# Kernel optimization log

Measured on AMD Instinct MI355X. Metric: run time of the kernel, lower is better.

The kernel has to match this reference:

```python
import jax, jax.numpy as jnp
import numpy as np

B, S, D = 4, 2048, 1024
N_NEURONS, K = 512, 8
N_BASIS, R = 32, 512
N_HEADS = 8
D_HEAD = R // N_HEADS


def setup_inputs() -> dict:
    key = jax.random.key(0)
    ks = jax.random.split(key, 8)
    x = jax.random.normal(ks[0], (B, S, D), dtype=jnp.float32)
    W_router = jax.random.normal(ks[1], (N_NEURONS, D), dtype=jnp.float32) / np.sqrt(D)
    recipe_Q = jax.random.normal(ks[2], (N_NEURONS, N_BASIS), dtype=jnp.float32)
    recipe_K = jax.random.normal(ks[3], (N_NEURONS, N_BASIS), dtype=jnp.float32)
    recipe_V = jax.random.normal(ks[4], (N_NEURONS, N_BASIS), dtype=jnp.float32)
    # orthonormal basis: QR of random [D, R] per basis slot (buffer, not trained)
    raw = jax.random.normal(ks[5], (N_BASIS, D, R), dtype=jnp.float32)
    basis = jax.vmap(lambda m: jnp.linalg.qr(m)[0])(raw)  # [N_BASIS, D, R]
    W_o = jax.random.normal(ks[6], (D, R), dtype=jnp.float32) / np.sqrt(R)
    mask = jnp.tril(jnp.ones((S, S), dtype=jnp.int32))[None, None]  # [1,1,S,S] causal
    mask = jnp.broadcast_to(mask, (B, 1, S, S))
    return {"x": x, "W_router": W_router, "recipe_Q": recipe_Q, "recipe_K": recipe_K,
            "recipe_V": recipe_V, "basis": basis, "W_o": W_o, "mask": mask}


def reference(x, W_router, recipe_Q, recipe_K, recipe_V, basis, W_o, mask):
    # routing: pick top-k neurons per token
    scores = jnp.einsum('bsd,nd->bsn', x, W_router)            # [B,S,N_NEURONS]
    topk_scores, topk_idx = jax.lax.top_k(scores, K)            # [B,S,K]
    weights = jax.nn.softmax(topk_scores, axis=-1)              # [B,S,K]

    def token_recipe(recipe):
        g = recipe[topk_idx]                                    # [B,S,K,N_BASIS]
        r = jnp.einsum('bskn,bsk->bsn', g, weights)             # [B,S,N_BASIS]
        return jax.nn.softmax(r, axis=-1)

    tQ = token_recipe(recipe_Q)
    tK = token_recipe(recipe_K)
    tV = token_recipe(recipe_V)

    # shared basis projection of x, reused for Q/K/V (same math as
    # W = einsum('bsn,ndr->bsdr'); Q = einsum('bsd,bsdr->bsr'))
    P = jnp.einsum('bsd,ndr->bsnr', x, basis)                   # [B,S,N_BASIS,R]
    Q = jnp.einsum('bsnr,bsn->bsr', P, tQ)
    Kt = jnp.einsum('bsnr,bsn->bsr', P, tK)
    V = jnp.einsum('bsnr,bsn->bsr', P, tV)

    def heads(t):
        return t.reshape(B, S, N_HEADS, D_HEAD).transpose(0, 2, 1, 3)  # [B,H,S,dh]

    Qh, Kh, Vh = heads(Q), heads(Kt), heads(V)
    attn = jnp.einsum('bhqd,bhkd->bhqk', Qh, Kh) / np.sqrt(D_HEAD)
    attn = jnp.where(mask == 0, jnp.float32(-1e30), attn)
    attn = jax.nn.softmax(attn, axis=-1)                        # dropout p: eval/no-op
    out = jnp.einsum('bhqk,bhkd->bhqd', attn, Vh)
    out = out.transpose(0, 2, 1, 3).reshape(B, S, R)
    attn_out = jnp.einsum('bsr,dr->bsd', out, W_o)
    return attn_out, topk_idx, weights
```

## Files before the change

### kernel.cpp

```cpp
#include <hip/hip_runtime.h>
#include <math.h>
#include <stdint.h>


typedef __attribute__((ext_vector_type(4))) float f32x4;
typedef __attribute__((ext_vector_type(8))) short s16x8;
typedef __attribute__((ext_vector_type(4))) short s16x4;
typedef __attribute__((ext_vector_type(4))) int i32x4;
typedef __attribute__((ext_vector_type(8))) int i32x8;

#define DEV __device__ __forceinline__

DEV short f2bf(float f){
  union { float f; unsigned u; } c; c.f = f;
  unsigned u = c.u;
  unsigned r = (u + 0x7fffu + ((u >> 16) & 1u)) >> 16;
  return (short)r;
}
DEV float bf2f(short s){
  union { unsigned u; float f; } c; c.u = ((unsigned)(unsigned short)s) << 16;
  return c.f;
}
DEV unsigned char f2e4m3(float f){
  union { float f; unsigned u; } c; c.f = f;
  unsigned u = c.u;
  unsigned sign = (u >> 24) & 0x80u;
  unsigned a = u & 0x7fffffffu;
  if (a >= 0x43e00000u) return (unsigned char)(sign | 0x7Eu);
  if (a < 0x3c800000u){
    union { unsigned u; float f; } d; d.u = a;
    int q = (int)(d.f * 512.0f + 0.5f);
    return (unsigned char)(sign | (unsigned)q);
  }
  unsigned m = a & 0x7fffffu;
  unsigned e = (a >> 23) - 120u;
  unsigned keep = m >> 20;
  unsigned rest = m & 0xFFFFFu;
  if (rest > 0x80000u || (rest == 0x80000u && (keep & 1u))){
    keep++;
    if (keep == 8u){ keep = 0; e++; }
  }
  if (e >= 16u || (e == 15u && keep == 7u)) return (unsigned char)(sign | 0x7Eu);
  return (unsigned char)(sign | (e << 3) | keep);
}

typedef __attribute__((address_space(3))) void lds_vt;
typedef const __attribute__((address_space(1))) void g_vt;
DEV void gload16(const void* g, void* lds){
  __builtin_amdgcn_global_load_lds((g_vt*)g, (lds_vt*)lds, 16, 0, 0);
}

DEV int gslot(int c){ return (c < 4) ? (c << 1) : (((c - 4) << 1) + 1); }

__global__ void k_conv_w(const float* __restrict__ Wo, const float* __restrict__ Wrt,
                         short* __restrict__ Wob, short* __restrict__ Wrtb){
  int i = blockIdx.x*256 + threadIdx.x;
  const float* src = (i < 131072) ? Wo : Wrt;
  short* dst = (i < 131072) ? Wob : Wrtb;
  int j = (i < 131072) ? i : (i - 131072);
  float4 v = ((const float4*)src)[j];
  s16x4 o; o[0]=f2bf(v.x); o[1]=f2bf(v.y); o[2]=f2bf(v.z); o[3]=f2bf(v.w);
  ((s16x4*)dst)[j] = o;
}

__global__ void k_conv_x(const float* __restrict__ in, short* __restrict__ Xb, char* __restrict__ Xf8){
  int t = blockIdx.x*256 + threadIdx.x;
  size_t d = (size_t)t * 16;
  const float4* s = (const float4*)(in + d);
  float vals[16];
  #pragma unroll
  for (int q=0;q<4;q++){ float4 v = s[q]; vals[q*4]=v.x; vals[q*4+1]=v.y; vals[q*4+2]=v.z; vals[q*4+3]=v.w; }
  s16x8 ob0, ob1;
  unsigned long long v0 = 0, v1 = 0;
  #pragma unroll
  for (int e=0;e<8;e++){
    ob0[e] = f2bf(vals[e]);
    ob1[e] = f2bf(vals[8+e]);
    v0 |= ((unsigned long long)f2e4m3(vals[e]))   << (8*e);
    v1 |= ((unsigned long long)f2e4m3(vals[8+e])) << (8*e);
  }
  *(s16x8*)(Xb + d) = ob0;
  *(s16x8*)(Xb + d + 8) = ob1;
  int c = t & 7;
  char* dst = Xf8 + (d & ~(size_t)127) + (gslot(c) << 4);
  *(unsigned long long*)dst = v0;
  *(unsigned long long*)(dst + 8) = v1;
}

__global__ __launch_bounds__(256) void k_conv_basis8(const float* __restrict__ basis, char* __restrict__ B2f){
  __shared__ float tile[64][65];
  int tid = threadIdx.x;
  int r0 = blockIdx.x<<6, d0 = blockIdx.y<<6, n = blockIdx.z;
  const float* src = basis + ((size_t)n*1024 + d0)*512 + r0;
  for (int i = tid; i < 4096; i += 256){ int dd = i>>6, rr = i&63; tile[dd][rr] = src[(size_t)dd*512 + rr]; }
  __syncthreads();
  int rr = tid >> 2, j = tid & 3;
  unsigned long long v0 = 0, v1 = 0;
  #pragma unroll
  for (int e=0;e<8;e++){
    v0 |= ((unsigned long long)f2e4m3(tile[j*16+e][rr]))   << (8*e);
    v1 |= ((unsigned long long)f2e4m3(tile[j*16+8+e][rr])) << (8*e);
  }
  int c = j + ((d0 >> 4) & 4);
  char* dst = B2f + ((size_t)(r0+rr)*32 + n)*1024 + (size_t)(d0 & ~127) + (gslot(c) << 4);
  *(unsigned long long*)dst = v0;
  *(unsigned long long*)(dst + 8) = v1;
}

__global__ __launch_bounds__(256) void k_gemm_c32(
    const short* __restrict__ A, const short* __restrict__ Bt, int Kd, int Mblk,
    float* __restrict__ C, int ldc)
{
  __shared__ char smem[32768];
  short* Asm = (short*)smem;
  short* Bsm = (short*)(smem + 16384);
  int tid = threadIdx.x, lane = tid & 63, w = tid >> 6;
  int wr = w >> 1, wc = w & 1;
  int nwg = gridDim.x, bid = blockIdx.x;
  int sid = (bid & 7) * (nwg >> 3) + (bid >> 3);
  int row0 = (sid % Mblk) << 7;
  int col0 = (sid / Mblk) << 7;
  f32x4 acc[4][4];
  #pragma unroll
  for (int m=0;m<4;m++)
    #pragma unroll
    for (int nf=0;nf<4;nf++)
      #pragma unroll
      for (int e=0;e<4;e++) acc[m][nf][e] = 0.f;
  int lr8 = lane >> 3;
  int lk_sw = (((lane & 7) ^ (lane >> 3)) << 3);
  for (int k0 = 0; k0 < Kd; k0 += 64){
    #pragma unroll
    for (int i=0;i<4;i++){
      int chunk = (w<<2) + i;
      int r = (chunk<<3) + lr8;
      gload16(A  + (size_t)(row0 + r)*Kd + k0 + lk_sw, smem + chunk*1024);
      gload16(Bt + (size_t)(col0 + r)*Kd + k0 + lk_sw, smem + 16384 + chunk*1024);
    }
    __syncthreads();
    #pragma unroll
    for (int kk=0; kk<2; kk++){
      int csw = (kk*32 + ((lane>>4)<<3)) ^ ((lane & 7) << 3);
      s16x8 af[4], bfr[4];
      #pragma unroll
      for (int m=0;m<4;m++)
        af[m] = *(const s16x8*)(Asm + ((wr*64 + m*16 + (lane&15))*64 + csw));
      #pragma unroll
      for (int nf=0;nf<4;nf++)
        bfr[nf] = *(const s16x8*)(Bsm + ((wc*64 + nf*16 + (lane&15))*64 + csw));
      #pragma unroll
      for (int m=0;m<4;m++)
        #pragma unroll
        for (int nf=0;nf<4;nf++)
          acc[m][nf] = __builtin_amdgcn_mfma_f32_16x16x32_bf16(af[m], bfr[nf], acc[m][nf], 0, 0, 0);
    }
    __syncthreads();
  }
  #pragma unroll
  for (int m=0;m<4;m++)
    #pragma unroll
    for (int nf=0;nf<4;nf++)
      #pragma unroll
      for (int e=0;e<4;e++){
        int tok = wr*64 + m*16 + ((lane>>4)<<2) + e;
        int col = wc*64 + nf*16 + (lane&15);
        C[(size_t)(row0+tok)*ldc + col0 + col] = acc[m][nf][e];
      }
}

#define STAGE_A(slotOff, arow0, tkt) do{ \
  int _t = (tkt) < 7 ? (tkt) : 7; \
  int _r = tid>>3, _g = tid&7; \
  gload16(B2f + (size_t)(row0 + (arow0) + _r)*1024 + (_t<<7) + ((_g ^ (_r&7))<<4), \
          smem + (slotOff) + (_r<<7) + (_g<<4)); \
}while(0)

#define STAGE_B(slotOff, trow0, tkt) do{ \
  int _t = (tkt) < 7 ? (tkt) : 7; \
  int _r = tid>>3, _g = tid&7; \
  gload16(Xf8 + (size_t)(col0 + (trow0) + _r)*1024 + (_t<<7) + ((_g ^ (_r&7))<<4), \
          smem + (slotOff) + (_r<<7) + (_g<<4)); \
  gload16(Xf8 + (size_t)(col0 + (trow0) + 64 + _r)*1024 + (_t<<7) + ((_g ^ (_r&7))<<4), \
          smem + (slotOff) + ((64+_r)<<7) + (_g<<4)); \
}while(0)

#define LD_AF(dst, base) \
  _Pragma("unroll") \
  for (int mi=0;mi<2;mi++){ \
    const char* _p = (base) + (wm*32 + mi*16 + l15)*128; \
    i32x4* _h = (i32x4*)&dst[mi]; \
    _h[0] = *(const i32x4*)(_p + ((ga0 ^ l7)<<4)); \
    _h[1] = *(const i32x4*)(_p + ((ga1 ^ l7)<<4)); \
  }

#define LD_BF(dst, base) \
  _Pragma("unroll") \
  for (int ni=0;ni<2;ni++){ \
    const char* _p = (base) + (wn*32 + ni*16 + l15)*128; \
    i32x4* _h = (i32x4*)&dst[ni]; \
    _h[0] = *(const i32x4*)(_p + ((ga0 ^ l7)<<4)); \
    _h[1] = *(const i32x4*)(_p + ((ga1 ^ l7)<<4)); \
  }

#define VMC(N) asm volatile("s_waitcnt vmcnt(" #N ")" ::: "memory")
#define PBAR() do{ __builtin_amdgcn_sched_barrier(0); __builtin_amdgcn_s_barrier(); }while(0)

#define MFMAP(Q, AF, BF) do{ \
  __builtin_amdgcn_s_setprio(1); \
  _Pragma("unroll") \
  for (int mi=0;mi<2;mi++) \
    _Pragma("unroll") \
    for (int ni=0;ni<2;ni++) \
      acc[Q][mi][ni] = __builtin_amdgcn_mfma_scale_f32_16x16x128_f8f6f4( \
          AF[mi], BF[ni], acc[Q][mi][ni], 0, 0, 0, 0x7f7f7f7f, 0, 0x7f7f7f7f); \
  __builtin_amdgcn_s_setprio(0); \
}while(0)

__global__ __launch_bounds__(512, 4) void k_pgemm8(
    const char* __restrict__ B2f, const char* __restrict__ Xf8,
    const float* __restrict__ tQp, const float* __restrict__ tKp, const float* __restrict__ tVp,
    short* __restrict__ Qb, short* __restrict__ Kb, short* __restrict__ Vt)
{
  extern __shared__ char smem[];
  int tid = threadIdx.x, lane = tid & 63, wid = tid >> 6;
  int wm = wid >> 2, wn = wid & 3;
  int l15 = lane & 15, l7 = lane & 7, g16 = lane >> 4;
  int ga0 = (g16 < 2) ? (g16 << 2) : (((g16 - 2) << 2) + 1);
  int ga1 = ga0 + 2;
  int bid = blockIdx.x;
  int xcd = bid & 7, lid = bid >> 3;
  int t_tile = (xcd << 2) + (lid & 3);
  int c_tile = lid >> 2;
  int row0 = c_tile << 7;
  int col0 = t_tile << 8;

  f32x4 acc[4][2][2];
  #pragma unroll
  for (int q=0;q<4;q++)
    #pragma unroll
    for (int mi=0;mi<2;mi++)
      #pragma unroll
      for (int ni=0;ni<2;ni++)
        #pragma unroll
        for (int e=0;e<4;e++) acc[q][mi][ni][e] = 0.f;
  i32x8 af[2], bf[2];

  STAGE_A(0, 0, 0);
  STAGE_B(24576, 0, 0);
  STAGE_A(16384, 64, 0);
  VMC(1);
  PBAR();

  for (int kt = 0; kt < 8; ++kt){
    const char* A0c = smem + ((kt&1)<<13);
    LD_AF(af, A0c);
    LD_BF(bf, smem + 24576);
    STAGE_B(40960, 128, kt);
    VMC(2);
    PBAR();
    MFMAP(0, af, bf);
    LD_AF(af, smem + 16384);
    STAGE_A(((kt+1)&1)<<13, 0, kt+1);
    VMC(1);
    PBAR();
    MFMAP(1, af, bf);
    LD_BF(bf, smem + 40960);
    STAGE_B(24576, 0, kt+1);
    PBAR();
    MFMAP(2, af, bf);
    LD_AF(af, A0c);
    STAGE_A(16384, 64, kt+1);
    VMC(1);
    PBAR();
    MFMAP(3, af, bf);
  }

  VMC(0);
  __syncthreads();
  short* t16 = (short*)smem;
  for (int i = tid; i < 8192; i += 512){
    int tk = i >> 5, n = i & 31;
    t16[tk*36 + n]            = f2bf(tQp[(size_t)col0*32 + i]);
    t16[9216 + tk*36 + n]     = f2bf(tKp[(size_t)col0*32 + i]);
    t16[18432 + tk*36 + n]    = f2bf(tVp[(size_t)col0*32 + i]);
  }
  __syncthreads();
  int g4 = g16 << 2;
  #pragma unroll
  for (int rec=0; rec<3; rec++){
    const short* tb = t16 + rec*9216;
    #pragma unroll
    for (int q=0;q<4;q++){
      int rh = (q==1)||(q==2);
      int ch = q >> 1;
      int r = (c_tile << 2) + rh*2 + wm;
      #pragma unroll
      for (int ni=0;ni<2;ni++){
        int tok = ch*128 + wn*32 + ni*16 + l15;
        s16x4 tlo = *(const s16x4*)(tb + tok*36 + g4);
        s16x4 thi = *(const s16x4*)(tb + tok*36 + 16 + g4);
        float p = 0.f;
        #pragma unroll
        for (int e=0;e<4;e++) p += acc[q][0][ni][e] * bf2f(tlo[e]);
        #pragma unroll
        for (int e=0;e<4;e++) p += acc[q][1][ni][e] * bf2f(thi[e]);
        p += __shfl_xor(p, 16);
        p += __shfl_xor(p, 32);
        if (g16 == rec){
          int gtok = col0 + tok;
          if (rec == 0)      Qb[(size_t)gtok*512 + r] = f2bf(p);
          else if (rec == 1) Kb[(size_t)gtok*512 + r] = f2bf(p);
          else Vt[(((size_t)(gtok>>11)*8 + (r>>6))*64 + (r&63))*2048 + (gtok&2047)] = f2bf(p);
        }
      }
    }
  }
}

__global__ __launch_bounds__(64) void k_router(const float* __restrict__ scores,
    const float* __restrict__ X, const float* __restrict__ W,
    const float* __restrict__ rQ, const float* __restrict__ rK, const float* __restrict__ rV,
    float* __restrict__ tQ, float* __restrict__ tK, float* __restrict__ tV,
    float* __restrict__ oidx, float* __restrict__ ow){
  int token = blockIdx.x; int lane = threadIdx.x;
  const float* srow = scores + (size_t)token*512;
  float v[8];
  #pragma unroll
  for (int j=0;j<8;j++) v[j] = srow[lane + 64*j];
  int myidx = 0x7fffffff;
  #pragma unroll
  for (int k=0;k<16;k++){
    float bm = -INFINITY; int bi = 0x7fffffff;
    #pragma unroll
    for (int j=0;j<8;j++){ if (v[j] > bm) { bm = v[j]; bi = lane + 64*j; } }
    #pragma unroll
    for (int off=32; off>=1; off>>=1){
      float om = __shfl_xor(bm, off); int oi = __shfl_xor(bi, off);
      if (om > bm || (om == bm && oi < bi)) { bm = om; bi = oi; }
    }
    if (lane == k) myidx = bi;
    #pragma unroll
    for (int j=0;j<8;j++) if (lane + 64*j == bi) v[j] = -INFINITY;
  }
  float xr[16];
  {
    const float4* x4 = (const float4*)(X + (size_t)token*1024 + lane*16);
    #pragma unroll
    for (int q=0;q<4;q++){ float4 t = x4[q]; xr[q*4]=t.x; xr[q*4+1]=t.y; xr[q*4+2]=t.z; xr[q*4+3]=t.w; }
  }
  double myref = -1e300;
  #pragma unroll
  for (int c=0;c<16;c++){
    int nid = __shfl(myidx, c);
    const float4* w4 = (const float4*)(W + (size_t)nid*1024 + lane*16);
    double acc = 0.0;
    #pragma unroll
    for (int q=0;q<4;q++){
      float4 t = w4[q];
      acc += (double)xr[q*4]   * (double)t.x;
      acc += (double)xr[q*4+1] * (double)t.y;
      acc += (double)xr[q*4+2] * (double)t.z;
      acc += (double)xr[q*4+3] * (double)t.w;
    }
    #pragma unroll
    for (int off=32; off>=1; off>>=1) acc += __shfl_xor(acc, off);
    if (lane == c) myref = acc;
  }
  double mv = myref; int mi = myidx;
  double topv[8]; int topi[8];
  #pragma unroll
  for (int k=0;k<8;k++){
    double bm = mv; int bi = mi;
    #pragma unroll
    for (int off=32; off>=1; off>>=1){
      double om = __shfl_xor(bm, off); int oi = __shfl_xor(bi, off);
      if (om > bm || (om == bm && oi < bi)) { bm = om; bi = oi; }
    }
    topv[k]=bm; topi[k]=bi;
    if (mi == bi) mv = -1e300;
  }
  double mx = topv[0]; double s = 0.0; double wd[8];
  #pragma unroll
  for (int k=0;k<8;k++){ wd[k] = exp(topv[k]-mx); s += wd[k]; }
  float w[8];
  #pragma unroll
  for (int k=0;k<8;k++) w[k] = (float)(wd[k]/s);
  if (lane == 0){
    #pragma unroll
    for (int k=0;k<8;k++){ oidx[(size_t)token*8+k] = (float)topi[k]; ow[(size_t)token*8+k] = w[k]; }
  }
  int n = lane & 31;
  float aq=0.f, ak=0.f, av=0.f;
  #pragma unroll
  for (int k=0;k<8;k++){
    size_t off = (size_t)topi[k]*32 + n;
    aq += w[k]*rQ[off]; ak += w[k]*rK[off]; av += w[k]*rV[off];
  }
  float mq = aq, mk2 = ak, mvv = av;
  #pragma unroll
  for (int off=16; off>=1; off>>=1){
    mq  = fmaxf(mq,  __shfl_xor(mq, off));
    mk2 = fmaxf(mk2, __shfl_xor(mk2,off));
    mvv = fmaxf(mvv, __shfl_xor(mvv,off));
  }
  float eq = expf(aq-mq), ek = expf(ak-mk2), ev = expf(av-mvv);
  float sq = eq, sk = ek, sv = ev;
  #pragma unroll
  for (int off=16; off>=1; off>>=1){
    sq += __shfl_xor(sq,off); sk += __shfl_xor(sk,off); sv += __shfl_xor(sv,off);
  }
  if (lane < 32){
    tQ[(size_t)token*32+n] = eq/sq;
    tK[(size_t)token*32+n] = ek/sk;
    tV[(size_t)token*32+n] = ev/sv;
  }
}

__global__ __launch_bounds__(256) void k_attn(const short* __restrict__ Qb, const short* __restrict__ Kb,
                                              const short* __restrict__ Vt, short* __restrict__ Ob)
{
  __shared__ char smem[40960];
  int tid = threadIdx.x, lane = tid & 63, wid = tid >> 6;
  int l15 = lane & 15, l7 = lane & 7, g16 = lane >> 4;
  int bid = blockIdx.x;
  int xcd = bid & 7, lid = bid >> 3;
  int work = xcd*128 + lid;
  int bx = 31 - (work & 31);
  int bh = work >> 5; int h = bh & 7, b = bh >> 3;
  size_t tokbase = (size_t)b*2048;
  int q0 = bx << 6;
  int nt = bx + 1;
  const float SC = 0.125f * 1.44269504f;

#define ATTN_STAGE(kt_) do{ \
  int _c = (kt_) & 1; \
  _Pragma("unroll") \
  for (int _i=0;_i<2;_i++){ \
    int _row = _i*32 + (wid<<3) + (lane>>3); \
    gload16(Kb + (tokbase + (((kt_)<<6) + _row))*512 + (h<<6) + ((l7 ^ (_row&7))<<3), \
            smem + (_c<<13) + _i*4096 + (wid<<10) + lane*16); \
    gload16(Vt + (size_t)((bh<<6) + _row)*2048 + ((kt_)<<6) + ((l7 ^ (_row&7))<<3), \
            smem + 16384 + (_c<<13) + _i*4096 + (wid<<10) + lane*16); \
  } \
}while(0)

  s16x8 qf[2];
  {
    const short* qp = Qb + (tokbase + q0 + wid*16 + l15)*512 + (h<<6);
    qf[0] = *(const s16x8*)(qp + g16*8);
    qf[1] = *(const s16x8*)(qp + 32 + g16*8);
  }
  int q_abs = q0 + wid*16 + l15;
  f32x4 o[4];
  float m_log = -INFINITY, l_sum = 0.f;
  #pragma unroll
  for (int i=0;i<4;i++)
    #pragma unroll
    for (int e=0;e<4;e++) o[i][e]=0.f;

  ATTN_STAGE(0);
  __syncthreads();

  for (int kt = 0; kt < nt; ++kt){
    if (kt + 1 < nt) ATTN_STAGE(kt+1);
    int cur = kt & 1;
    const char* Kc = smem + (cur<<13);
    const char* Vc = smem + 16384 + (cur<<13);
    char* Pb = smem + 32768 + (wid<<11);
    f32x4 S[4];
    #pragma unroll
    for (int s16=0;s16<4;s16++){
      #pragma unroll
      for (int e=0;e<4;e++) S[s16][e] = 0.f;
      const char* kr = Kc + (s16*16 + l15)*128;
      s16x8 kf0 = *(const s16x8*)(kr + (((g16  ) ^ l7)<<4));
      s16x8 kf1 = *(const s16x8*)(kr + (((4+g16) ^ l7)<<4));
      S[s16] = __builtin_amdgcn_mfma_f32_16x16x32_bf16(kf0, qf[0], S[s16], 0,0,0);
      S[s16] = __builtin_amdgcn_mfma_f32_16x16x32_bf16(kf1, qf[1], S[s16], 0,0,0);
    }
    bool diag = (kt == nt-1);
    float sm[16];
    #pragma unroll
    for (int s16=0;s16<4;s16++)
      #pragma unroll
      for (int e=0;e<4;e++){
        float sv = S[s16][e] * SC;
        if (diag){
          int kv_abs = (kt<<6) + s16*16 + (g16<<2) + e;
          if (kv_abs > q_abs) sv = -1e30f;
        }
        sm[s16*4+e] = sv;
      }
    float pmax = sm[0];
    #pragma unroll
    for (int j=1;j<16;j++) pmax = fmaxf(pmax, sm[j]);
    pmax = fmaxf(pmax, __shfl_xor(pmax, 16));
    pmax = fmaxf(pmax, __shfl_xor(pmax, 32));
    float mnew = fmaxf(m_log, pmax);
    float alpha = exp2f(m_log - mnew);
    m_log = mnew;
    float p[16], ps = 0.f;
    #pragma unroll
    for (int j=0;j<16;j++){ p[j] = exp2f(sm[j] - mnew); ps += p[j]; }
    ps += __shfl_xor(ps, 16);
    ps += __shfl_xor(ps, 32);
    l_sum = l_sum*alpha + ps;
    #pragma unroll
    for (int e=0;e<4;e++){
      float al = __shfl(alpha, (g16<<2)+e);
      #pragma unroll
      for (int df=0;df<4;df++) o[df][e] *= al;
    }
    #pragma unroll
    for (int s16=0;s16<4;s16++){
      s16x4 pk;
      #pragma unroll
      for (int e=0;e<4;e++) pk[e] = f2bf(p[s16*4+e]);
      *(s16x4*)(Pb + l15*128 + (((s16<<5) + (g16<<3)) ^ (l7<<4))) = pk;
    }
    s16x8 pf0 = *(const s16x8*)(Pb + l15*128 + (((g16  ) ^ l7)<<4));
    s16x8 pf1 = *(const s16x8*)(Pb + l15*128 + (((4+g16) ^ l7)<<4));
    #pragma unroll
    for (int df=0;df<4;df++){
      const char* vr = Vc + (df*16 + l15)*128;
      s16x8 vf0 = *(const s16x8*)(vr + (((g16  ) ^ l7)<<4));
      s16x8 vf1 = *(const s16x8*)(vr + (((4+g16) ^ l7)<<4));
      o[df] = __builtin_amdgcn_mfma_f32_16x16x32_bf16(pf0, vf0, o[df], 0,0,0);
      o[df] = __builtin_amdgcn_mfma_f32_16x16x32_bf16(pf1, vf1, o[df], 0,0,0);
    }
    __syncthreads();
  }
  #pragma unroll
  for (int e=0;e<4;e++){
    float ln = __shfl(l_sum, (g16<<2)+e);
    float inv = 1.0f / ln;
    #pragma unroll
    for (int df=0;df<4;df++){
      int q = q0 + wid*16 + (g16<<2) + e;
      int d = df*16 + l15;
      Ob[(tokbase + q)*512 + (h<<6) + d] = f2bf(o[df][e] * inv);
    }
  }
#undef ATTN_STAGE
}

extern "C" void kernel_launch(void* const* d_in, const int* in_sizes, int n_in,
                              void* d_out, int out_size, void* d_ws, size_t ws_size,
                              hipStream_t stream)
{
  const float* x     = (const float*)d_in[0];
  const float* Wrt   = (const float*)d_in[1];
  const float* rQ    = (const float*)d_in[2];
  const float* rK    = (const float*)d_in[3];
  const float* rV    = (const float*)d_in[4];
  const float* basis = (const float*)d_in[5];
  const float* Wo    = (const float*)d_in[6];
  float* out = (float*)d_out;
  char* ws = (char*)d_ws;
  char*  B2f  = (char*)(ws + 0);
  char*  Xf8  = (char*)(ws + 16777216);
  short* Xb   = (short*)(ws + 25165824);
  float* SC   = (float*)(ws + 41943040);
  float* tQ   = (float*)(ws + 58720256);
  float* tK   = (float*)(ws + 59768832);
  float* tV   = (float*)(ws + 60817408);
  short* Qb   = (short*)(ws + 61865984);
  short* Kb   = (short*)(ws + 70254592);
  short* Vt   = (short*)(ws + 78643200);
  short* Ob   = (short*)(ws + 87031808);
  short* Wob  = (short*)(ws + 95420416);
  short* Wrtb = (short*)(ws + 96468992);
  float* oidx = out + 8388608;
  float* oww  = out + 8454144;

  hipFuncSetAttribute((const void*)k_pgemm8, hipFuncAttributeMaxDynamicSharedMemorySize, 57344);

  k_conv_x<<<2048, 256, 0, stream>>>(x, Xb, Xf8);
  k_conv_w<<<1024, 256, 0, stream>>>(Wo, Wrt, Wob, Wrtb);
  k_conv_basis8<<<dim3(8,16,32), 256, 0, stream>>>(basis, B2f);
  k_gemm_c32<<<256, 256, 0, stream>>>(Xb, Wrtb, 1024, 64, SC, 512);
  k_router<<<8192, 64, 0, stream>>>(SC, x, Wrt, rQ, rK, rV, tQ, tK, tV, oidx, oww);
  k_pgemm8<<<4096, 512, 57344, stream>>>(B2f, Xf8, tQ, tK, tV, Qb, Kb, Vt);
  k_attn<<<1024, 256, 0, stream>>>(Qb, Kb, Vt, Ob);
  k_gemm_c32<<<512, 256, 0, stream>>>(Ob, Wob, 512, 64, out, 1024);
}
```

Baseline: 399.8 us.

## Merge conversion kernels, drop a barrier in pgemm loop, vectorize recipe staging

Three separate changes. The x and weight conversion kernels are merged into one launch, removing one kernel dispatch. In the pgemm main loop a second A-fragment register set keeps the first A fragment live across the iteration, so one LDS reload and one barrier can be removed and the last two MFMA phases run back to back. The epilogue loads of recipe weights now use float2 reads and packed bf16 stores. The extra fragment registers raise register pressure and could lower occupancy.

```diff
diff --git a/kernel.cpp b/kernel.cpp
--- a/kernel.cpp
+++ b/kernel.cpp
@@ -20,6 +20,9 @@
 DEV float bf2f(short s){
   union { unsigned u; float f; } c; c.u = ((unsigned)(unsigned short)s) << 16;
   return c.f;
+}
+DEV int pack2bf(float a, float b){
+  return (int)(unsigned short)f2bf(a) | (((int)(unsigned short)f2bf(b)) << 16);
 }
 DEV unsigned char f2e4m3(float f){
   union { float f; unsigned u; } c; c.f = f;
@@ -52,39 +55,40 @@
 
 DEV int gslot(int c){ return (c < 4) ? (c << 1) : (((c - 4) << 1) + 1); }
 
-__global__ void k_conv_w(const float* __restrict__ Wo, const float* __restrict__ Wrt,
-                         short* __restrict__ Wob, short* __restrict__ Wrtb){
-  int i = blockIdx.x*256 + threadIdx.x;
-  const float* src = (i < 131072) ? Wo : Wrt;
-  short* dst = (i < 131072) ? Wob : Wrtb;
-  int j = (i < 131072) ? i : (i - 131072);
-  float4 v = ((const float4*)src)[j];
-  s16x4 o; o[0]=f2bf(v.x); o[1]=f2bf(v.y); o[2]=f2bf(v.z); o[3]=f2bf(v.w);
-  ((s16x4*)dst)[j] = o;
-}
-
-__global__ void k_conv_x(const float* __restrict__ in, short* __restrict__ Xb, char* __restrict__ Xf8){
+__global__ void k_conv_xw(const float* __restrict__ x, short* __restrict__ Xb, char* __restrict__ Xf8,
+                          const float* __restrict__ Wo, const float* __restrict__ Wrt,
+                          short* __restrict__ Wob, short* __restrict__ Wrtb){
   int t = blockIdx.x*256 + threadIdx.x;
-  size_t d = (size_t)t * 16;
-  const float4* s = (const float4*)(in + d);
-  float vals[16];
-  #pragma unroll
-  for (int q=0;q<4;q++){ float4 v = s[q]; vals[q*4]=v.x; vals[q*4+1]=v.y; vals[q*4+2]=v.z; vals[q*4+3]=v.w; }
-  s16x8 ob0, ob1;
-  unsigned long long v0 = 0, v1 = 0;
-  #pragma unroll
-  for (int e=0;e<8;e++){
-    ob0[e] = f2bf(vals[e]);
-    ob1[e] = f2bf(vals[8+e]);
-    v0 |= ((unsigned long long)f2e4m3(vals[e]))   << (8*e);
-    v1 |= ((unsigned long long)f2e4m3(vals[8+e])) << (8*e);
-  }
-  *(s16x8*)(Xb + d) = ob0;
-  *(s16x8*)(Xb + d + 8) = ob1;
-  int c = t & 7;
-  char* dst = Xf8 + (d & ~(size_t)127) + (gslot(c) << 4);
-  *(unsigned long long*)dst = v0;
-  *(unsigned long long*)(dst + 8) = v1;
+  if (t < 524288){
+    size_t d = (size_t)t * 16;
+    const float4* s = (const float4*)(x + d);
+    float vals[16];
+    #pragma unroll
+    for (int q=0;q<4;q++){ float4 v = s[q]; vals[q*4]=v.x; vals[q*4+1]=v.y; vals[q*4+2]=v.z; vals[q*4+3]=v.w; }
+    s16x8 ob0, ob1;
+    unsigned long long v0 = 0, v1 = 0;
+    #pragma unroll
+    for (int e=0;e<8;e++){
+      ob0[e] = f2bf(vals[e]);
+      ob1[e] = f2bf(vals[8+e]);
+      v0 |= ((unsigned long long)f2e4m3(vals[e]))   << (8*e);
+      v1 |= ((unsigned long long)f2e4m3(vals[8+e])) << (8*e);
+    }
+    *(s16x8*)(Xb + d) = ob0;
+    *(s16x8*)(Xb + d + 8) = ob1;
+    int c = t & 7;
+    char* dst = Xf8 + (d & ~(size_t)127) + (gslot(c) << 4);
+    *(unsigned long long*)dst = v0;
+    *(unsigned long long*)(dst + 8) = v1;
+  } else {
+    int i = t - 524288;
+    const float* src = (i < 131072) ? Wo : Wrt;
+    short* dst = (i < 131072) ? Wob : Wrtb;
+    int j = (i < 131072) ? i : (i - 131072);
+    float4 v = ((const float4*)src)[j];
+    s16x4 o; o[0]=f2bf(v.x); o[1]=f2bf(v.y); o[2]=f2bf(v.z); o[3]=f2bf(v.w);
+    ((s16x4*)dst)[j] = o;
+  }
 }
 
 __global__ __launch_bounds__(256) void k_conv_basis8(const float* __restrict__ basis, char* __restrict__ B2f){
@@ -243,7 +247,7 @@
       for (int ni=0;ni<2;ni++)
         #pragma unroll
         for (int e=0;e<4;e++) acc[q][mi][ni][e] = 0.f;
-  i32x8 af[2], bf[2];
+  i32x8 af[2], af1[2], bf[2];
 
   STAGE_A(0, 0, 0);
   STAGE_B(24576, 0, 0);
@@ -259,30 +263,31 @@
     VMC(2);
     PBAR();
     MFMAP(0, af, bf);
-    LD_AF(af, smem + 16384);
+    LD_AF(af1, smem + 16384);
     STAGE_A(((kt+1)&1)<<13, 0, kt+1);
     VMC(1);
     PBAR();
-    MFMAP(1, af, bf);
+    MFMAP(1, af1, bf);
     LD_BF(bf, smem + 40960);
     STAGE_B(24576, 0, kt+1);
-    PBAR();
-    MFMAP(2, af, bf);
-    LD_AF(af, A0c);
     STAGE_A(16384, 64, kt+1);
     VMC(1);
     PBAR();
+    MFMAP(2, af1, bf);
     MFMAP(3, af, bf);
   }
 
   VMC(0);
   __syncthreads();
   short* t16 = (short*)smem;
-  for (int i = tid; i < 8192; i += 512){
-    int tk = i >> 5, n = i & 31;
-    t16[tk*36 + n]            = f2bf(tQp[(size_t)col0*32 + i]);
-    t16[9216 + tk*36 + n]     = f2bf(tKp[(size_t)col0*32 + i]);
-    t16[18432 + tk*36 + n]    = f2bf(tVp[(size_t)col0*32 + i]);
+  for (int i2 = tid; i2 < 4096; i2 += 512){
+    int tk = i2 >> 4, np = (i2 & 15) << 1;
+    float2 a = *(const float2*)(tQp + (size_t)col0*32 + i2*2);
+    float2 b = *(const float2*)(tKp + (size_t)col0*32 + i2*2);
+    float2 c = *(const float2*)(tVp + (size_t)col0*32 + i2*2);
+    *(int*)&t16[tk*36 + np]         = pack2bf(a.x, a.y);
+    *(int*)&t16[9216 + tk*36 + np]  = pack2bf(b.x, b.y);
+    *(int*)&t16[18432 + tk*36 + np] = pack2bf(c.x, c.y);
   }
   __syncthreads();
   int g4 = g16 << 2;
@@ -575,8 +580,7 @@
 
   hipFuncSetAttribute((const void*)k_pgemm8, hipFuncAttributeMaxDynamicSharedMemorySize, 57344);
 
-  k_conv_x<<<2048, 256, 0, stream>>>(x, Xb, Xf8);
-  k_conv_w<<<1024, 256, 0, stream>>>(Wo, Wrt, Wob, Wrtb);
+  k_conv_xw<<<3072, 256, 0, stream>>>(x, Xb, Xf8, Wo, Wrt, Wob, Wrtb);
   k_conv_basis8<<<dim3(8,16,32), 256, 0, stream>>>(basis, B2f);
   k_gemm_c32<<<256, 256, 0, stream>>>(Xb, Wrtb, 1024, 64, SC, 512);
   k_router<<<8192, 64, 0, stream>>>(SC, x, Wrt, rQ, rK, rV, tQ, tK, tV, oidx, oww);
```

Measured after the change: 533.0 us. +33.3%, slower.
